# Optimization experiments

Measured on AMD Instinct MI355X. Metric: run time of the kernel, lower is better.

The kernel has to match this reference:

```python
import jax, jax.numpy as jnp
import numpy as np

N_RAW, N1, N2, K, D, OUT = 200000, 100000, 20000, 10, 256, 256

def setup_inputs() -> dict:
    key = jax.random.key(0)
    ks = jax.random.split(key, 8)
    scale1 = (6.0 / (OUT + 2 * D)) ** 0.5   # xavier_uniform bound
    scale2 = (6.0 / (OUT + 2 * OUT)) ** 0.5
    return {
        "raw_features": jax.random.normal(ks[0], (N_RAW, D), dtype=jnp.float32),
        "W1": jax.random.uniform(ks[1], (OUT, 2 * D), jnp.float32, -scale1, scale1),
        "W2": jax.random.uniform(ks[2], (OUT, 2 * OUT), jnp.float32, -scale2, scale2),
        "nodes1": jax.random.randint(ks[3], (N1,), 0, N_RAW),
        "neigh1": jax.random.randint(ks[4], (N1, K), 0, N_RAW),
        "self2": jax.random.randint(ks[5], (N2,), 0, N1),
        "neigh2": jax.random.randint(ks[6], (N2, K), 0, N1),
    }

def _sage_layer(embs, self_idx, neigh_idx, W):
    # segment-mean over sampled neighbors (MEAN agg with fixed fanout K)
    agg = jnp.mean(embs[neigh_idx], axis=1)          # [n, d]
    combined = jnp.concatenate([embs[self_idx], agg], axis=1)  # [n, 2d]
    # F.relu(W.mm(combined.t())).t() == relu(combined @ W.T)
    return jax.nn.relu(combined @ W.T)

def reference(raw_features, W1, W2, nodes1, neigh1, self2, neigh2):
    h1 = _sage_layer(raw_features, nodes1, neigh1, W1)  # [N1, OUT]
    h2 = _sage_layer(h1, self2, neigh2, W2)             # [N2, OUT]
    return h2
```

## Files before the change

### kernel.cpp

```cpp
#include <hip/hip_runtime.h>
#include <hip/hip_bf16.h>


typedef __attribute__((ext_vector_type(8))) short bf16x8;
typedef __attribute__((ext_vector_type(4))) float f32x4;

static __device__ __forceinline__ short f2bf(float f) {
  __hip_bfloat16 h = __float2bfloat16(f);
  return *reinterpret_cast<short*>(&h);
}
static __device__ __forceinline__ float bf2f(short s) {
  union { unsigned u; float f; } x;
  x.u = ((unsigned)(unsigned short)s) << 16;
  return x.f;
}

__global__ __launch_bounds__(256) void convert_all(
    const float* __restrict__ raw, const float* __restrict__ W1,
    const float* __restrict__ W2, short* __restrict__ rawb,
    short* __restrict__ W1b, short* __restrict__ W2b) {
  const int b = blockIdx.x;
  const float* src;
  short* dst;
  size_t base;
  if (b < 25000) { src = raw; dst = rawb; base = (size_t)b * 2048; }
  else if (b < 25064) { src = W1; dst = W1b; base = (size_t)(b - 25000) * 2048; }
  else { src = W2; dst = W2b; base = (size_t)(b - 25064) * 2048; }
  const size_t i = base + (size_t)threadIdx.x * 8;
  const f32x4* s4 = reinterpret_cast<const f32x4*>(src + i);
  f32x4 u = __builtin_nontemporal_load(s4);
  f32x4 v = __builtin_nontemporal_load(s4 + 1);
  bf16x8 o;
  o[0] = f2bf(u.x); o[1] = f2bf(u.y); o[2] = f2bf(u.z); o[3] = f2bf(u.w);
  o[4] = f2bf(v.x); o[5] = f2bf(v.y); o[6] = f2bf(v.z); o[7] = f2bf(v.w);
  *reinterpret_cast<bf16x8*>(dst + i) = o;
}

template <bool OUT_BF16>
__global__ __launch_bounds__(512, 8) void sage_fused(
    const short* __restrict__ E,
    const int* __restrict__ self_idx,
    const int* __restrict__ neigh,
    const short* __restrict__ Wb,
    void* __restrict__ out) {
  __shared__ short As[32][520];

  const int tid = threadIdx.x;
  const int m0 = blockIdx.x * 32;
  const int c = tid & 31;
  const int rs = tid >> 5;

#pragma unroll
  for (int rr = 0; rr < 2; ++rr) {
    const int r = rs * 2 + rr;
    const int gr = m0 + r;
    const int si = self_idx[gr];
    int nbx[10];
#pragma unroll
    for (int k = 0; k < 10; ++k) nbx[k] = neigh[gr * 10 + k];
    bf16x8 sv = *reinterpret_cast<const bf16x8*>(E + (size_t)si * 256 + c * 8);
    bf16x8 v[10];
#pragma unroll
    for (int k = 0; k < 10; ++k)
      v[k] = *reinterpret_cast<const bf16x8*>(E + (size_t)nbx[k] * 256 + c * 8);
    bf16x8 mv;
#pragma unroll
    for (int j = 0; j < 8; ++j) {
      float sA = bf2f(v[0][j]) + bf2f(v[2][j]) + bf2f(v[4][j]) + bf2f(v[6][j]) + bf2f(v[8][j]);
      float sB = bf2f(v[1][j]) + bf2f(v[3][j]) + bf2f(v[5][j]) + bf2f(v[7][j]) + bf2f(v[9][j]);
      mv[j] = f2bf((sA + sB) * 0.1f);
    }
    *reinterpret_cast<bf16x8*>(&As[r][c * 8]) = sv;
    *reinterpret_cast<bf16x8*>(&As[r][256 + c * 8]) = mv;
  }
  __syncthreads();

  const int wave = tid >> 6, lane = tid & 63;
  const int wn = wave * 32;
  const int lr = lane & 15;
  const int lkb = (lane >> 4) * 8;
  const short* Bp = Wb + (size_t)(wn + lr) * 512 + lkb;

  f32x4 acc[2][2] = {};

#pragma unroll
  for (int ks = 0; ks < 16; ++ks) {
    const int k0 = ks * 32;
    bf16x8 a0 = *reinterpret_cast<const bf16x8*>(&As[lr][k0 + lkb]);
    bf16x8 a1 = *reinterpret_cast<const bf16x8*>(&As[16 + lr][k0 + lkb]);
    bf16x8 b0 = *reinterpret_cast<const bf16x8*>(Bp + k0);
    bf16x8 b1 = *reinterpret_cast<const bf16x8*>(Bp + k0 + 8192);
    __builtin_amdgcn_s_setprio(1);
    acc[0][0] = __builtin_amdgcn_mfma_f32_16x16x32_bf16(a0, b0, acc[0][0], 0, 0, 0);
    acc[1][0] = __builtin_amdgcn_mfma_f32_16x16x32_bf16(a1, b0, acc[1][0], 0, 0, 0);
    acc[0][1] = __builtin_amdgcn_mfma_f32_16x16x32_bf16(a0, b1, acc[0][1], 0, 0, 0);
    acc[1][1] = __builtin_amdgcn_mfma_f32_16x16x32_bf16(a1, b1, acc[1][1], 0, 0, 0);
    __builtin_amdgcn_s_setprio(0);
  }

#pragma unroll
  for (int mi = 0; mi < 2; ++mi)
#pragma unroll
    for (int ni = 0; ni < 2; ++ni)
#pragma unroll
      for (int r = 0; r < 4; ++r) {
        const int gm = m0 + mi * 16 + (lane >> 4) * 4 + r;
        const int gn = wn + ni * 16 + lr;
        float v = acc[mi][ni][r];
        v = v > 0.f ? v : 0.f;
        if (OUT_BF16)
          reinterpret_cast<short*>(out)[(size_t)gm * 256 + gn] = f2bf(v);
        else
          reinterpret_cast<float*>(out)[(size_t)gm * 256 + gn] = v;
      }
}

extern "C" void kernel_launch(void* const* d_in, const int* in_sizes, int n_in,
                              void* d_out, int out_size, void* d_ws, size_t ws_size,
                              hipStream_t stream) {
  const float* raw = (const float*)d_in[0];
  const float* W1 = (const float*)d_in[1];
  const float* W2 = (const float*)d_in[2];
  const int* nodes1 = (const int*)d_in[3];
  const int* neigh1 = (const int*)d_in[4];
  const int* self2 = (const int*)d_in[5];
  const int* neigh2 = (const int*)d_in[6];
  float* out = (float*)d_out;

  const int N_RAW = 200000, N1 = 100000;

  short* rawb = (short*)d_ws;
  short* h1 = rawb + (size_t)N_RAW * 256;
  short* W1b = h1 + (size_t)N1 * 256;
  short* W2b = W1b + 131072;

  convert_all<<<25128, 256, 0, stream>>>(raw, W1, W2, rawb, W1b, W2b);
  sage_fused<true><<<3125, 512, 0, stream>>>(rawb, nodes1, neigh1, W1b, h1);
  sage_fused<false><<<625, 512, 0, stream>>>(h1, self2, neigh2, W2b, out);
}
```

Measured before the change: 226.4 us.

## Make SAGE kernels persistent with double-buffered gather overlapping MFMA compute

Replaces one-block-per-32-row-tile launches with a persistent grid of 512 blocks, each looping over a contiguous range of tiles. The LDS A tile is double-buffered: while MFMAs run on the current tile, the next tile's neighbor gathers are issued and reduced into the other buffer, and indices two tiles ahead are prefetched. The aim is to hide gather latency behind matrix compute. In exchange it doubles LDS, holds more registers for in-flight vectors, lowers occupancy (launch bounds 4), and leaves the 625-tile second layer with only about one tile per block.

```diff
diff --git a/kernel.cpp b/kernel.cpp
--- a/kernel.cpp
+++ b/kernel.cpp
@@ -37,43 +37,23 @@
 }
 
 template <bool OUT_BF16>
-__global__ __launch_bounds__(512, 8) void sage_fused(
+__global__ __launch_bounds__(512, 4) void sage_pipe(
     const short* __restrict__ E,
     const int* __restrict__ self_idx,
     const int* __restrict__ neigh,
     const short* __restrict__ Wb,
-    void* __restrict__ out) {
-  __shared__ short As[32][520];
+    void* __restrict__ out,
+    int ntiles) {
+  __shared__ short As[2][32][520];
 
   const int tid = threadIdx.x;
-  const int m0 = blockIdx.x * 32;
+  const int nblk = gridDim.x;
+  const int start = (int)(((long long)blockIdx.x * ntiles) / nblk);
+  const int end = (int)(((long long)(blockIdx.x + 1) * ntiles) / nblk);
+  if (start >= end) return;
+
   const int c = tid & 31;
   const int rs = tid >> 5;
-
-#pragma unroll
-  for (int rr = 0; rr < 2; ++rr) {
-    const int r = rs * 2 + rr;
-    const int gr = m0 + r;
-    const int si = self_idx[gr];
-    int nbx[10];
-#pragma unroll
-    for (int k = 0; k < 10; ++k) nbx[k] = neigh[gr * 10 + k];
-    bf16x8 sv = *reinterpret_cast<const bf16x8*>(E + (size_t)si * 256 + c * 8);
-    bf16x8 v[10];
-#pragma unroll
-    for (int k = 0; k < 10; ++k)
-      v[k] = *reinterpret_cast<const bf16x8*>(E + (size_t)nbx[k] * 256 + c * 8);
-    bf16x8 mv;
-#pragma unroll
-    for (int j = 0; j < 8; ++j) {
-      float sA = bf2f(v[0][j]) + bf2f(v[2][j]) + bf2f(v[4][j]) + bf2f(v[6][j]) + bf2f(v[8][j]);
-      float sB = bf2f(v[1][j]) + bf2f(v[3][j]) + bf2f(v[5][j]) + bf2f(v[7][j]) + bf2f(v[9][j]);
-      mv[j] = f2bf((sA + sB) * 0.1f);
-    }
-    *reinterpret_cast<bf16x8*>(&As[r][c * 8]) = sv;
-    *reinterpret_cast<bf16x8*>(&As[r][256 + c * 8]) = mv;
-  }
-  __syncthreads();
 
   const int wave = tid >> 6, lane = tid & 63;
   const int wn = wave * 32;
@@ -81,38 +61,119 @@
   const int lkb = (lane >> 4) * 8;
   const short* Bp = Wb + (size_t)(wn + lr) * 512 + lkb;
 
-  f32x4 acc[2][2] = {};
-
-#pragma unroll
-  for (int ks = 0; ks < 16; ++ks) {
-    const int k0 = ks * 32;
-    bf16x8 a0 = *reinterpret_cast<const bf16x8*>(&As[lr][k0 + lkb]);
-    bf16x8 a1 = *reinterpret_cast<const bf16x8*>(&As[16 + lr][k0 + lkb]);
-    bf16x8 b0 = *reinterpret_cast<const bf16x8*>(Bp + k0);
-    bf16x8 b1 = *reinterpret_cast<const bf16x8*>(Bp + k0 + 8192);
-    __builtin_amdgcn_s_setprio(1);
-    acc[0][0] = __builtin_amdgcn_mfma_f32_16x16x32_bf16(a0, b0, acc[0][0], 0, 0, 0);
-    acc[1][0] = __builtin_amdgcn_mfma_f32_16x16x32_bf16(a1, b0, acc[1][0], 0, 0, 0);
-    acc[0][1] = __builtin_amdgcn_mfma_f32_16x16x32_bf16(a0, b1, acc[0][1], 0, 0, 0);
-    acc[1][1] = __builtin_amdgcn_mfma_f32_16x16x32_bf16(a1, b1, acc[1][1], 0, 0, 0);
-    __builtin_amdgcn_s_setprio(0);
+  auto load_idx = [&](int t, int rr, int* nbx, int& six)
+      __attribute__((always_inline)) {
+    const int gr = t * 32 + rs * 2 + rr;
+#pragma unroll
+    for (int k = 0; k < 10; ++k) nbx[k] = neigh[gr * 10 + k];
+    six = self_idx[gr];
+  };
+  auto issue_feat = [&](const int* nbx, int six, bf16x8* v)
+      __attribute__((always_inline)) {
+#pragma unroll
+    for (int k = 0; k < 10; ++k)
+      v[k] = *reinterpret_cast<const bf16x8*>(E + (size_t)(unsigned)nbx[k] * 256 + c * 8);
+    v[10] = *reinterpret_cast<const bf16x8*>(E + (size_t)(unsigned)six * 256 + c * 8);
+  };
+  auto reduce_write = [&](int rr, int buf, const bf16x8* v)
+      __attribute__((always_inline)) {
+    const int r = rs * 2 + rr;
+    bf16x8 mv;
+#pragma unroll
+    for (int j = 0; j < 8; ++j) {
+      float sA = bf2f(v[0][j]) + bf2f(v[2][j]) + bf2f(v[4][j]) + bf2f(v[6][j]) + bf2f(v[8][j]);
+      float sB = bf2f(v[1][j]) + bf2f(v[3][j]) + bf2f(v[5][j]) + bf2f(v[7][j]) + bf2f(v[9][j]);
+      mv[j] = f2bf((sA + sB) * 0.1f);
+    }
+    *reinterpret_cast<bf16x8*>(&As[buf][r][c * 8]) = v[10];
+    *reinterpret_cast<bf16x8*>(&As[buf][r][256 + c * 8]) = mv;
+  };
+
+  bf16x8 vs[11];
+  int nbxN[10], sixN;
+
+#pragma unroll
+  for (int rr = 0; rr < 2; ++rr) {
+    int nbx[10], six;
+    load_idx(start, rr, nbx, six);
+    bf16x8 v[11];
+    issue_feat(nbx, six, v);
+    reduce_write(rr, 0, v);
   }
-
-#pragma unroll
-  for (int mi = 0; mi < 2; ++mi)
-#pragma unroll
-    for (int ni = 0; ni < 2; ++ni)
-#pragma unroll
-      for (int r = 0; r < 4; ++r) {
-        const int gm = m0 + mi * 16 + (lane >> 4) * 4 + r;
-        const int gn = wn + ni * 16 + lr;
-        float v = acc[mi][ni][r];
-        v = v > 0.f ? v : 0.f;
-        if (OUT_BF16)
-          reinterpret_cast<short*>(out)[(size_t)gm * 256 + gn] = f2bf(v);
-        else
-          reinterpret_cast<float*>(out)[(size_t)gm * 256 + gn] = v;
-      }
+  if (start + 1 < end) {
+    int nbx0[10], six0;
+    load_idx(start + 1, 0, nbx0, six0);
+    issue_feat(nbx0, six0, vs);
+    load_idx(start + 1, 1, nbxN, sixN);
+  }
+  __syncthreads();
+
+  for (int t = start; t < end; ++t) {
+    const int buf = (t - start) & 1;
+    const bool hn = (t + 1 < end);
+    const bool hn2 = (t + 2 < end);
+    f32x4 acc[2][2] = {};
+
+#pragma unroll
+    for (int ks = 0; ks < 8; ++ks) {
+      bf16x8 a0 = *reinterpret_cast<const bf16x8*>(&As[buf][lr][ks * 32 + lkb]);
+      bf16x8 a1 = *reinterpret_cast<const bf16x8*>(&As[buf][16 + lr][ks * 32 + lkb]);
+      bf16x8 b0 = *reinterpret_cast<const bf16x8*>(Bp + ks * 32);
+      bf16x8 b1 = *reinterpret_cast<const bf16x8*>(Bp + ks * 32 + 8192);
+      __builtin_amdgcn_s_setprio(1);
+      acc[0][0] = __builtin_amdgcn_mfma_f32_16x16x32_bf16(a0, b0, acc[0][0], 0, 0, 0);
+      acc[1][0] = __builtin_amdgcn_mfma_f32_16x16x32_bf16(a1, b0, acc[1][0], 0, 0, 0);
+      acc[0][1] = __builtin_amdgcn_mfma_f32_16x16x32_bf16(a0, b1, acc[0][1], 0, 0, 0);
+      acc[1][1] = __builtin_amdgcn_mfma_f32_16x16x32_bf16(a1, b1, acc[1][1], 0, 0, 0);
+      __builtin_amdgcn_s_setprio(0);
+    }
+    __builtin_amdgcn_sched_barrier(0);
+    if (hn) {
+      reduce_write(0, buf ^ 1, vs);
+      issue_feat(nbxN, sixN, vs);
+    }
+    __builtin_amdgcn_sched_barrier(0);
+    if (hn2) load_idx(t + 2, 0, nbxN, sixN);
+    __builtin_amdgcn_sched_barrier(0);
+
+#pragma unroll
+    for (int ks = 8; ks < 16; ++ks) {
+      bf16x8 a0 = *reinterpret_cast<const bf16x8*>(&As[buf][lr][ks * 32 + lkb]);
+      bf16x8 a1 = *reinterpret_cast<const bf16x8*>(&As[buf][16 + lr][ks * 32 + lkb]);
+      bf16x8 b0 = *reinterpret_cast<const bf16x8*>(Bp + ks * 32);
+      bf16x8 b1 = *reinterpret_cast<const bf16x8*>(Bp + ks * 32 + 8192);
+      __builtin_amdgcn_s_setprio(1);
+      acc[0][0] = __builtin_amdgcn_mfma_f32_16x16x32_bf16(a0, b0, acc[0][0], 0, 0, 0);
+      acc[1][0] = __builtin_amdgcn_mfma_f32_16x16x32_bf16(a1, b0, acc[1][0], 0, 0, 0);
+      acc[0][1] = __builtin_amdgcn_mfma_f32_16x16x32_bf16(a0, b1, acc[0][1], 0, 0, 0);
+      acc[1][1] = __builtin_amdgcn_mfma_f32_16x16x32_bf16(a1, b1, acc[1][1], 0, 0, 0);
+      __builtin_amdgcn_s_setprio(0);
+    }
+    __builtin_amdgcn_sched_barrier(0);
+    if (hn) reduce_write(1, buf ^ 1, vs);
+    if (hn2) {
+      issue_feat(nbxN, sixN, vs);
+      load_idx(t + 2, 1, nbxN, sixN);
+    }
+    __builtin_amdgcn_sched_barrier(0);
+
+#pragma unroll
+    for (int mi = 0; mi < 2; ++mi)
+#pragma unroll
+      for (int ni = 0; ni < 2; ++ni)
+#pragma unroll
+        for (int r = 0; r < 4; ++r) {
+          const int gm = t * 32 + mi * 16 + (lane >> 4) * 4 + r;
+          const int gn = wn + ni * 16 + lr;
+          float v = acc[mi][ni][r];
+          v = v > 0.f ? v : 0.f;
+          if (OUT_BF16)
+            reinterpret_cast<short*>(out)[(size_t)gm * 256 + gn] = f2bf(v);
+          else
+            reinterpret_cast<float*>(out)[(size_t)gm * 256 + gn] = v;
+        }
+    __syncthreads();
+  }
 }
 
 extern "C" void kernel_launch(void* const* d_in, const int* in_sizes, int n_in,
@@ -135,6 +196,6 @@
   short* W2b = W1b + 131072;
 
   convert_all<<<25128, 256, 0, stream>>>(raw, W1, W2, rawb, W1b, W2b);
-  sage_fused<true><<<3125, 512, 0, stream>>>(rawb, nodes1, neigh1, W1b, h1);
-  sage_fused<false><<<625, 512, 0, stream>>>(h1, self2, neigh2, W2b, out);
-}
+  sage_pipe<true><<<512, 512, 0, stream>>>(rawb, nodes1, neigh1, W1b, h1, 3125);
+  sage_pipe<false><<<512, 512, 0, stream>>>(h1, self2, neigh2, W2b, out, 625);
+}
```

Result: slower. 317.6 us (+40.3%).

## Double rows per block to 64 and prefetch weight fragments across k-steps

Applied to the files above, without the earlier changes.

Each block now aggregates and multiplies 64 rows instead of 32. This halves the number of times each block reloads the full W matrix from global memory and doubles the MFMA work per weight fragment. The next k-step's B fragments are register-prefetched so global weight loads overlap the MFMAs. Tail handling (clamping row indices and a guarded store) is added because 100000 and 20000 are not multiples of 64. The costs are twice the LDS per block and more registers, with occupancy lowered to 4 blocks per CU in launch bounds, and fewer blocks in layer 2 (313).

```diff
diff --git a/kernel.cpp b/kernel.cpp
--- a/kernel.cpp
+++ b/kernel.cpp
@@ -37,32 +37,34 @@
 }
 
 template <bool OUT_BF16>
-__global__ __launch_bounds__(512, 8) void sage_fused(
+__global__ __launch_bounds__(512, 4) void sage_fused(
     const short* __restrict__ E,
     const int* __restrict__ self_idx,
     const int* __restrict__ neigh,
     const short* __restrict__ Wb,
-    void* __restrict__ out) {
-  __shared__ short As[32][520];
+    void* __restrict__ out,
+    int Nvalid) {
+  __shared__ short As[64][520];
 
   const int tid = threadIdx.x;
-  const int m0 = blockIdx.x * 32;
+  const int m0 = blockIdx.x * 64;
   const int c = tid & 31;
   const int rs = tid >> 5;
 
 #pragma unroll
-  for (int rr = 0; rr < 2; ++rr) {
-    const int r = rs * 2 + rr;
-    const int gr = m0 + r;
+  for (int rr = 0; rr < 4; ++rr) {
+    const int r = rs * 4 + rr;
+    int gr = m0 + r;
+    gr = gr < Nvalid ? gr : Nvalid - 1;
     const int si = self_idx[gr];
     int nbx[10];
 #pragma unroll
     for (int k = 0; k < 10; ++k) nbx[k] = neigh[gr * 10 + k];
-    bf16x8 sv = *reinterpret_cast<const bf16x8*>(E + (size_t)si * 256 + c * 8);
+    bf16x8 sv = *reinterpret_cast<const bf16x8*>(E + (size_t)(unsigned)si * 256 + c * 8);
     bf16x8 v[10];
 #pragma unroll
     for (int k = 0; k < 10; ++k)
-      v[k] = *reinterpret_cast<const bf16x8*>(E + (size_t)nbx[k] * 256 + c * 8);
+      v[k] = *reinterpret_cast<const bf16x8*>(E + (size_t)(unsigned)nbx[k] * 256 + c * 8);
     bf16x8 mv;
 #pragma unroll
     for (int j = 0; j < 8; ++j) {
@@ -81,25 +83,37 @@
   const int lkb = (lane >> 4) * 8;
   const short* Bp = Wb + (size_t)(wn + lr) * 512 + lkb;
 
-  f32x4 acc[2][2] = {};
+  f32x4 acc[4][2] = {};
+
+  bf16x8 b0 = *reinterpret_cast<const bf16x8*>(Bp);
+  bf16x8 b1 = *reinterpret_cast<const bf16x8*>(Bp + 8192);
 
 #pragma unroll
   for (int ks = 0; ks < 16; ++ks) {
-    const int k0 = ks * 32;
-    bf16x8 a0 = *reinterpret_cast<const bf16x8*>(&As[lr][k0 + lkb]);
-    bf16x8 a1 = *reinterpret_cast<const bf16x8*>(&As[16 + lr][k0 + lkb]);
-    bf16x8 b0 = *reinterpret_cast<const bf16x8*>(Bp + k0);
-    bf16x8 b1 = *reinterpret_cast<const bf16x8*>(Bp + k0 + 8192);
+    bf16x8 nb0, nb1;
+    if (ks < 15) {
+      nb0 = *reinterpret_cast<const bf16x8*>(Bp + (ks + 1) * 32);
+      nb1 = *reinterpret_cast<const bf16x8*>(Bp + (ks + 1) * 32 + 8192);
+    }
+    bf16x8 a0 = *reinterpret_cast<const bf16x8*>(&As[lr][ks * 32 + lkb]);
+    bf16x8 a1 = *reinterpret_cast<const bf16x8*>(&As[16 + lr][ks * 32 + lkb]);
+    bf16x8 a2 = *reinterpret_cast<const bf16x8*>(&As[32 + lr][ks * 32 + lkb]);
+    bf16x8 a3 = *reinterpret_cast<const bf16x8*>(&As[48 + lr][ks * 32 + lkb]);
     __builtin_amdgcn_s_setprio(1);
     acc[0][0] = __builtin_amdgcn_mfma_f32_16x16x32_bf16(a0, b0, acc[0][0], 0, 0, 0);
     acc[1][0] = __builtin_amdgcn_mfma_f32_16x16x32_bf16(a1, b0, acc[1][0], 0, 0, 0);
+    acc[2][0] = __builtin_amdgcn_mfma_f32_16x16x32_bf16(a2, b0, acc[2][0], 0, 0, 0);
+    acc[3][0] = __builtin_amdgcn_mfma_f32_16x16x32_bf16(a3, b0, acc[3][0], 0, 0, 0);
     acc[0][1] = __builtin_amdgcn_mfma_f32_16x16x32_bf16(a0, b1, acc[0][1], 0, 0, 0);
     acc[1][1] = __builtin_amdgcn_mfma_f32_16x16x32_bf16(a1, b1, acc[1][1], 0, 0, 0);
+    acc[2][1] = __builtin_amdgcn_mfma_f32_16x16x32_bf16(a2, b1, acc[2][1], 0, 0, 0);
+    acc[3][1] = __builtin_amdgcn_mfma_f32_16x16x32_bf16(a3, b1, acc[3][1], 0, 0, 0);
     __builtin_amdgcn_s_setprio(0);
+    b0 = nb0; b1 = nb1;
   }
 
 #pragma unroll
-  for (int mi = 0; mi < 2; ++mi)
+  for (int mi = 0; mi < 4; ++mi)
 #pragma unroll
     for (int ni = 0; ni < 2; ++ni)
 #pragma unroll
@@ -108,10 +122,12 @@
         const int gn = wn + ni * 16 + lr;
         float v = acc[mi][ni][r];
         v = v > 0.f ? v : 0.f;
-        if (OUT_BF16)
-          reinterpret_cast<short*>(out)[(size_t)gm * 256 + gn] = f2bf(v);
-        else
-          reinterpret_cast<float*>(out)[(size_t)gm * 256 + gn] = v;
+        if (gm < Nvalid) {
+          if (OUT_BF16)
+            reinterpret_cast<short*>(out)[(size_t)gm * 256 + gn] = f2bf(v);
+          else
+            reinterpret_cast<float*>(out)[(size_t)gm * 256 + gn] = v;
+        }
       }
 }
 
@@ -127,7 +143,7 @@
   const int* neigh2 = (const int*)d_in[6];
   float* out = (float*)d_out;
 
-  const int N_RAW = 200000, N1 = 100000;
+  const int N_RAW = 200000, N1 = 100000, N2 = 20000;
 
   short* rawb = (short*)d_ws;
   short* h1 = rawb + (size_t)N_RAW * 256;
@@ -135,6 +151,6 @@
   short* W2b = W1b + 131072;
 
   convert_all<<<25128, 256, 0, stream>>>(raw, W1, W2, rawb, W1b, W2b);
-  sage_fused<true><<<3125, 512, 0, stream>>>(rawb, nodes1, neigh1, W1b, h1);
-  sage_fused<false><<<625, 512, 0, stream>>>(h1, self2, neigh2, W2b, out);
+  sage_fused<true><<<(N1 + 63) / 64, 512, 0, stream>>>(rawb, nodes1, neigh1, W1b, h1, N1);
+  sage_fused<false><<<(N2 + 63) / 64, 512, 0, stream>>>(h1, self2, neigh2, W2b, out, N2);
 }
```

After: 204.6 us (median of 2 runs). -9.6%, faster.
